# Kernel tuning notes

Hardware: AMD Instinct MI355X
Metric: run time of the kernel (lower is better)

## Reference

```python
import jax, jax.numpy as jnp
import numpy as np

AUG = 8     # augmented_dim
NSUB = 4    # fixed Bosh3 substeps per save interval (replaces adaptive PID controller)


def setup_inputs() -> dict:
    key = jax.random.key(0)
    ks = jax.random.split(key, 8)
    B, T, DATA, WIDTH = 256, 64, 256, 256
    D = DATA + AUG
    ts = jnp.linspace(0.0, 1.0, T, dtype=jnp.float32)
    xs = jax.random.uniform(ks[0], (B, DATA), dtype=jnp.float32)
    a_sample = jax.random.normal(ks[1], (B,), dtype=jnp.float32)

    def lin(k, fan_in, fan_out):
        lim = 1.0 / np.sqrt(fan_in)
        kw, kb = jax.random.split(k)
        W = jax.random.uniform(kw, (fan_out, fan_in), minval=-lim, maxval=lim, dtype=jnp.float32)
        b = jax.random.uniform(kb, (fan_out,), minval=-lim, maxval=lim, dtype=jnp.float32)
        return W, b

    W0, b0 = lin(ks[2], D, WIDTH)
    W1, b1 = lin(ks[3], WIDTH, WIDTH)
    W2, b2 = lin(ks[4], WIDTH, WIDTH)
    W3, b3 = lin(ks[5], WIDTH, D)
    return dict(ts=ts, xs=xs, a_sample=a_sample,
                W0=W0, b0=b0, W1=W1, b1=b1, W2=W2, b2=b2, W3=W3, b3=b3)


def reference(ts, xs, a_sample, W0, b0, W1, b1, W2, b2, W3, b3):
    B = xs.shape[0]

    def f(y):  # autonomous vector field: MLP(y), batched over B
        h = jnp.tanh(y @ W0.T + b0)
        h = jnp.tanh(h @ W1.T + b1)
        h = jnp.tanh(h @ W2.T + b2)
        return h @ W3.T + b3

    # y0 = concat(a * exp(-0.1*t0) * sin(pi*xs), zeros(AUG))
    u0 = jnp.sin(jnp.pi * xs)
    scale = (a_sample * jnp.exp(-0.1 * ts[0]))[:, None]
    y0 = jnp.concatenate([scale * u0, jnp.zeros((B, AUG), xs.dtype)], axis=-1)  # [B, D]

    @jax.checkpoint
    def bosh3_step(y, h):
        k1 = f(y)
        k2 = f(y + 0.5 * h * k1)
        k3 = f(y + 0.75 * h * k2)
        return y + h * ((2.0 / 9.0) * k1 + (1.0 / 3.0) * k2 + (4.0 / 9.0) * k3)

    def interval(y, dt):
        h = dt / NSUB
        y = jax.lax.fori_loop(0, NSUB, lambda i, yy: bosh3_step(yy, h), y)
        return y, y

    dts = ts[1:] - ts[:-1]
    _, ys_tail = jax.lax.scan(interval, y0, dts)             # [T-1, B, D]
    ys = jnp.concatenate([y0[None], ys_tail], axis=0)        # [T, B, D]
    ys = jnp.transpose(ys, (1, 0, 2))[..., :-AUG]            # [B, T, data_size]
    return ys
```

## Files before the change

kernel.cpp:

```cpp
#include <hip/hip_runtime.h>
#include <cmath>

#define NB   256
#define NT   64
#define DATA 256
#define DD   264
#define NSUB 4
#define NTH  1024
#define NW   16
#define PI_F 3.14159265358979323846f

typedef _Float16 h2 __attribute__((ext_vector_type(2)));
typedef __fp16   g2 __attribute__((ext_vector_type(2)));

#define WS_W0  0
#define WS_W1  (WS_W0 + 136 * 256)
#define WS_W2  (WS_W1 + 128 * 256)
#define WS_W3  (WS_W2 + 128 * 256)
#define WS_W3T (WS_W3 + 128 * 256)

#define L_W1   0
#define L_PS   (L_W1 + 128 * 256)
#define L_YP   (L_PS + NW * 272)
#define L_INP  (L_YP + 136)
#define L_HAP  (L_INP + 136)
#define L_HBP  (L_HAP + 128)
#define L_Y    (L_HBP + 128)
#define L_ACC  (L_Y + 272)
#define L_B0   (L_ACC + 272)
#define L_B1   (L_B0 + 256)
#define L_B2   (L_B1 + 256)
#define L_B3   (L_B2 + 256)
#define LDS_WORDS (L_B3 + 272)

__device__ __forceinline__ float dot2(unsigned wu, unsigned hu, float c) {
  h2 a = __builtin_bit_cast(h2, wu);
  h2 b = __builtin_bit_cast(h2, hu);
#if __has_builtin(__builtin_amdgcn_fdot2)
  return __builtin_amdgcn_fdot2(a, b, c, false);
#else
  return c + (float)a[0] * (float)b[0] + (float)a[1] * (float)b[1];
#endif
}

__device__ __forceinline__ unsigned pkh(float a, float b) {
#if __has_builtin(__builtin_amdgcn_cvt_pkrtz)
  g2 v = __builtin_amdgcn_cvt_pkrtz(a, b);
  return __builtin_bit_cast(unsigned, v);
#else
  h2 v; v[0] = (_Float16)a; v[1] = (_Float16)b;
  return __builtin_bit_cast(unsigned, v);
#endif
}

__device__ __forceinline__ unsigned pkh_rne(float a, float b) {
  h2 v; v[0] = (_Float16)a; v[1] = (_Float16)b;
  return __builtin_bit_cast(unsigned, v);
}

#define DOT4(acc, u, hp)                                                      \
  acc.x = dot2(u.x, hp, acc.x);                                               \
  acc.y = dot2(u.y, hp, acc.y);                                               \
  acc.z = dot2(u.z, hp, acc.z);                                               \
  acc.w = dot2(u.w, hp, acc.w);

__global__ void prep(const float* __restrict__ W0, const float* __restrict__ W1,
                     const float* __restrict__ W2, const float* __restrict__ W3,
                     unsigned* __restrict__ wsu) {
  int tid = blockIdx.x * blockDim.x + threadIdx.x;
  int stride = gridDim.x * blockDim.x;
  for (int i = tid; i < 136 * 256; i += stride) {
    int kk = i >> 8, j = i & 255;
    int k0 = 2 * kk, k1 = 2 * kk + 1;
    float lo = (k0 < DD) ? W0[j * DD + k0] : 0.f;
    float hi = (k1 < DD) ? W0[j * DD + k1] : 0.f;
    wsu[WS_W0 + i] = pkh_rne(lo, hi);
  }
  for (int i = tid; i < 128 * 256; i += stride) {
    int kk = i >> 8, j = i & 255;
    wsu[WS_W1 + i] = pkh_rne(W1[j * 256 + 2 * kk], W1[j * 256 + 2 * kk + 1]);
    wsu[WS_W2 + i] = pkh_rne(W2[j * 256 + 2 * kk], W2[j * 256 + 2 * kk + 1]);
    wsu[WS_W3 + i] = pkh_rne(W3[j * 256 + 2 * kk], W3[j * 256 + 2 * kk + 1]);
  }
  for (int i = tid; i < 128 * 16; i += stride) {
    int kk = i >> 4, c = 256 + (i & 15);
    float lo = (c < DD) ? W3[c * 256 + 2 * kk] : 0.f;
    float hi = (c < DD) ? W3[c * 256 + 2 * kk + 1] : 0.f;
    wsu[WS_W3T + i] = pkh_rne(lo, hi);
  }
}

__global__ __launch_bounds__(NTH) void node_integrate(
    const float* __restrict__ ts, const float* __restrict__ xs,
    const float* __restrict__ a_sample,
    const float* __restrict__ b0g, const float* __restrict__ b1g,
    const float* __restrict__ b2g, const float* __restrict__ b3g,
    const unsigned* __restrict__ wsu, float* __restrict__ out) {
  extern __shared__ float sm[];
  unsigned* smu = (unsigned*)sm;
  const int b   = blockIdx.x;
  const int tid = threadIdx.x;
  const int w   = tid >> 6;
  const int l   = tid & 63;

  for (int i = tid; i < 256; i += NTH) {
    sm[L_B0 + i] = b0g[i];
    sm[L_B1 + i] = b1g[i];
    sm[L_B2 + i] = b2g[i];
  }
  for (int i = tid; i < 272; i += NTH) sm[L_B3 + i] = (i < DD) ? b3g[i] : 0.f;
  {
    const uint4* src = (const uint4*)(wsu + WS_W1);
    uint4* dst = (uint4*)(smu + L_W1);
    for (int i = tid; i < 128 * 64; i += NTH) dst[i] = src[i];
  }
  {
    const float sc = a_sample[b] * expf(-0.1f * ts[0]);
    for (int i = tid; i < 272; i += NTH) {
      float v = 0.f;
      if (i < DATA) v = sc * sinf(PI_F * xs[(size_t)b * DATA + i]);
      sm[L_Y + i] = v;
    }
  }
  __syncthreads();
  if (tid < 136) {
    smu[L_YP + tid]  = pkh(sm[L_Y + 2 * tid], sm[L_Y + 2 * tid + 1]);
    smu[L_INP + tid] = 0u;
  }
  __syncthreads();

  if (tid < DATA) out[((size_t)b * NT) * DATA + tid] = sm[L_Y + tid];

  float4* ps4 = (float4*)(sm + L_PS);
  const uint4* w0b4 = (const uint4*)(wsu + WS_W0);
  const uint4* w2b4 = (const uint4*)(wsu + WS_W2);
  const uint4* w3b4 = (const uint4*)(wsu + WS_W3);
  const uint4* w3t4 = (const uint4*)(wsu + WS_W3T);
  const uint4* w1l4 = (const uint4*)(smu + L_W1);

#pragma unroll 1
  for (int t = 0; t < NT - 1; ++t) {
    const float dt = ts[t + 1] - ts[t];
    const float h  = dt * (1.0f / NSUB);
#pragma unroll 1
    for (int sub = 0; sub < NSUB; ++sub) {
#pragma unroll 1
      for (int st = 0; st < 3; ++st) {
        const unsigned* finp = smu + ((st == 0) ? L_YP : L_INP);

        {
          float4 acc; acc.x = acc.y = acc.z = acc.w = 0.f;
#pragma unroll 4
          for (int i = 0; i < 8; ++i) {
            const int kk = w + 16 * i;
            const uint4 u = w0b4[kk * 64 + l];
            const unsigned hp = finp[kk];
            DOT4(acc, u, hp)
          }
          if (w < 8) {
            const int kk = 128 + w;
            const uint4 u = w0b4[kk * 64 + l];
            const unsigned hp = finp[kk];
            DOT4(acc, u, hp)
          }
          ps4[w * 68 + l] = acc;
        }
        __syncthreads();
        if (tid < 256) {
          float sv = sm[L_B0 + tid];
#pragma unroll
          for (int ww = 0; ww < NW; ++ww) sv += sm[L_PS + ww * 272 + tid];
          const float hv = tanhf(sv);
          const float ho = __shfl_xor(hv, 1);
          if (!(tid & 1)) smu[L_HAP + (tid >> 1)] = pkh(hv, ho);
        }
        __syncthreads();

        {
          float4 acc; acc.x = acc.y = acc.z = acc.w = 0.f;
#pragma unroll 4
          for (int i = 0; i < 8; ++i) {
            const int kk = w + 16 * i;
            const uint4 u = w1l4[kk * 64 + l];
            const unsigned hp = smu[L_HAP + kk];
            DOT4(acc, u, hp)
          }
          ps4[w * 68 + l] = acc;
        }
        __syncthreads();
        if (tid < 256) {
          float sv = sm[L_B1 + tid];
#pragma unroll
          for (int ww = 0; ww < NW; ++ww) sv += sm[L_PS + ww * 272 + tid];
          const float hv = tanhf(sv);
          const float ho = __shfl_xor(hv, 1);
          if (!(tid & 1)) smu[L_HBP + (tid >> 1)] = pkh(hv, ho);
        }
        __syncthreads();

        {
          float4 acc; acc.x = acc.y = acc.z = acc.w = 0.f;
#pragma unroll 4
          for (int i = 0; i < 8; ++i) {
            const int kk = w + 16 * i;
            const uint4 u = w2b4[kk * 64 + l];
            const unsigned hp = smu[L_HBP + kk];
            DOT4(acc, u, hp)
          }
          ps4[w * 68 + l] = acc;
        }
        __syncthreads();
        if (tid < 256) {
          float sv = sm[L_B2 + tid];
#pragma unroll
          for (int ww = 0; ww < NW; ++ww) sv += sm[L_PS + ww * 272 + tid];
          const float hv = tanhf(sv);
          const float ho = __shfl_xor(hv, 1);
          if (!(tid & 1)) smu[L_HAP + (tid >> 1)] = pkh(hv, ho);
        }
        __syncthreads();

        {
          float4 acc; acc.x = acc.y = acc.z = acc.w = 0.f;
#pragma unroll 4
          for (int i = 0; i < 8; ++i) {
            const int kk = w + 16 * i;
            const uint4 u = w3b4[kk * 64 + l];
            const unsigned hp = smu[L_HAP + kk];
            DOT4(acc, u, hp)
          }
          ps4[w * 68 + l] = acc;
          if (l < 4) {
            float4 accx; accx.x = accx.y = accx.z = accx.w = 0.f;
#pragma unroll 4
            for (int i = 0; i < 8; ++i) {
              const int kk = w + 16 * i;
              const uint4 u = w3t4[kk * 4 + l];
              const unsigned hp = smu[L_HAP + kk];
              DOT4(accx, u, hp)
            }
            ps4[w * 68 + 64 + l] = accx;
          }
        }
        __syncthreads();
        if (tid < DD) {
          float kv = sm[L_B3 + tid];
#pragma unroll
          for (int ww = 0; ww < NW; ++ww) kv += sm[L_PS + ww * 272 + tid];
          float val;
          if (st == 0) {
            sm[L_ACC + tid] = (2.0f / 9.0f) * kv;
            val = sm[L_Y + tid] + 0.5f * h * kv;
          } else if (st == 1) {
            sm[L_ACC + tid] += (1.0f / 3.0f) * kv;
            val = sm[L_Y + tid] + 0.75f * h * kv;
          } else {
            val = sm[L_Y + tid] + h * (sm[L_ACC + tid] + (4.0f / 9.0f) * kv);
            sm[L_Y + tid] = val;
          }
          const float vo = __shfl_xor(val, 1);
          if (!(tid & 1)) {
            const int dst = (st == 2) ? L_YP : L_INP;
            smu[dst + (tid >> 1)] = pkh(val, vo);
          }
        }
        __syncthreads();
      }
    }
    if (tid < DATA) out[((size_t)b * NT + (t + 1)) * DATA + tid] = sm[L_Y + tid];
  }
}

extern "C" void kernel_launch(void* const* d_in, const int* in_sizes, int n_in,
                              void* d_out, int out_size, void* d_ws, size_t ws_size,
                              hipStream_t stream) {
  const float* ts = (const float*)d_in[0];
  const float* xs = (const float*)d_in[1];
  const float* a  = (const float*)d_in[2];
  const float* W0 = (const float*)d_in[3];
  const float* b0 = (const float*)d_in[4];
  const float* W1 = (const float*)d_in[5];
  const float* b1 = (const float*)d_in[6];
  const float* W2 = (const float*)d_in[7];
  const float* b2 = (const float*)d_in[8];
  const float* W3 = (const float*)d_in[9];
  const float* b3 = (const float*)d_in[10];
  unsigned* ws = (unsigned*)d_ws;
  float* out = (float*)d_out;

  const size_t lds_bytes = LDS_WORDS * sizeof(float);
  (void)hipFuncSetAttribute(reinterpret_cast<const void*>(node_integrate),
                            hipFuncAttributeMaxDynamicSharedMemorySize,
                            (int)lds_bytes);

  hipLaunchKernelGGL(prep, dim3(256), dim3(256), 0, stream, W0, W1, W2, W3, ws);
  hipLaunchKernelGGL(node_integrate, dim3(NB), dim3(NTH), lds_bytes, stream,
                     ts, xs, a, b0, b1, b2, b3, ws, out);
}
```

Baseline: 4.697 ms.

## Keep ODE state in registers and align each wave's K-slice to its own outputs

Each wave now reduces the outputs it will consume as the K-slice of the next layer, so the tanh-and-pack step no longer needs a block-wide barrier. This roughly halves __syncthreads per MLP evaluation. Partial sums are double-buffered between two LDS regions. The RK state (y, acc) and biases move into registers, and the augmented tail is handled by a small separate path. To make room in LDS, the last rows of W1 are now read from global memory. That adds some global traffic and branching in the W1 loop.

```diff
diff --git a/kernel.cpp b/kernel.cpp
--- a/kernel.cpp
+++ b/kernel.cpp
@@ -7,7 +7,6 @@
 #define DD   264
 #define NSUB 4
 #define NTH  1024
-#define NW   16
 #define PI_F 3.14159265358979323846f
 
 typedef _Float16 h2 __attribute__((ext_vector_type(2)));
@@ -19,19 +18,13 @@
 #define WS_W3  (WS_W2 + 128 * 256)
 #define WS_W3T (WS_W3 + 128 * 256)
 
+#define NW1LDS 124
 #define L_W1   0
-#define L_PS   (L_W1 + 128 * 256)
-#define L_YP   (L_PS + NW * 272)
-#define L_INP  (L_YP + 136)
-#define L_HAP  (L_INP + 136)
-#define L_HBP  (L_HAP + 128)
-#define L_Y    (L_HBP + 128)
-#define L_ACC  (L_Y + 272)
-#define L_B0   (L_ACC + 272)
-#define L_B1   (L_B0 + 256)
-#define L_B2   (L_B1 + 256)
-#define L_B3   (L_B2 + 256)
-#define LDS_WORDS (L_B3 + 272)
+#define L_PSA  (L_W1 + NW1LDS * 256)
+#define L_PSB  (L_PSA + 16 * 256)
+#define L_PT   (L_PSB + 16 * 256)
+#define L_FPH  (L_PT + 16 * 8)
+#define LDS_WORDS (L_FPH + 16 * 9)
 
 __device__ __forceinline__ float dot2(unsigned wu, unsigned hu, float c) {
   h2 a = __builtin_bit_cast(h2, wu);
@@ -42,7 +35,6 @@
   return c + (float)a[0] * (float)b[0] + (float)a[1] * (float)b[1];
 #endif
 }
-
 __device__ __forceinline__ unsigned pkh(float a, float b) {
 #if __has_builtin(__builtin_amdgcn_cvt_pkrtz)
   g2 v = __builtin_amdgcn_cvt_pkrtz(a, b);
@@ -52,7 +44,6 @@
   return __builtin_bit_cast(unsigned, v);
 #endif
 }
-
 __device__ __forceinline__ unsigned pkh_rne(float a, float b) {
   h2 v; v[0] = (_Float16)a; v[1] = (_Float16)b;
   return __builtin_bit_cast(unsigned, v);
@@ -82,11 +73,9 @@
     wsu[WS_W2 + i] = pkh_rne(W2[j * 256 + 2 * kk], W2[j * 256 + 2 * kk + 1]);
     wsu[WS_W3 + i] = pkh_rne(W3[j * 256 + 2 * kk], W3[j * 256 + 2 * kk + 1]);
   }
-  for (int i = tid; i < 128 * 16; i += stride) {
-    int kk = i >> 4, c = 256 + (i & 15);
-    float lo = (c < DD) ? W3[c * 256 + 2 * kk] : 0.f;
-    float hi = (c < DD) ? W3[c * 256 + 2 * kk + 1] : 0.f;
-    wsu[WS_W3T + i] = pkh_rne(lo, hi);
+  for (int i = tid; i < 128 * 8; i += stride) {
+    int kk = i >> 3, c = 256 + (i & 7);
+    wsu[WS_W3T + i] = pkh_rne(W3[c * 256 + 2 * kk], W3[c * 256 + 2 * kk + 1]);
   }
 }
 
@@ -96,178 +85,185 @@
     const float* __restrict__ b0g, const float* __restrict__ b1g,
     const float* __restrict__ b2g, const float* __restrict__ b3g,
     const unsigned* __restrict__ wsu, float* __restrict__ out) {
-  extern __shared__ float sm[];
-  unsigned* smu = (unsigned*)sm;
-  const int b   = blockIdx.x;
+  HIP_DYNAMIC_SHARED(unsigned, sm);
+  float* smf = (float*)sm;
+  const int b = blockIdx.x;
   const int tid = threadIdx.x;
-  const int w   = tid >> 6;
-  const int l   = tid & 63;
-
-  for (int i = tid; i < 256; i += NTH) {
-    sm[L_B0 + i] = b0g[i];
-    sm[L_B1 + i] = b1g[i];
-    sm[L_B2 + i] = b2g[i];
-  }
-  for (int i = tid; i < 272; i += NTH) sm[L_B3 + i] = (i < DD) ? b3g[i] : 0.f;
+  const int w = tid >> 6, l = tid & 63;
+  const int g = l >> 2, s = l & 3;
+  const int jg = 16 * w + g;
+
   {
     const uint4* src = (const uint4*)(wsu + WS_W1);
-    uint4* dst = (uint4*)(smu + L_W1);
-    for (int i = tid; i < 128 * 64; i += NTH) dst[i] = src[i];
-  }
+    uint4* dst = (uint4*)(sm + L_W1);
+    for (int i = tid; i < NW1LDS * 64; i += NTH) dst[i] = src[i];
+  }
+  const float rb0 = b0g[jg], rb1 = b1g[jg], rb2 = b2g[jg], rb3 = b3g[jg];
+  const int jt = 256 + 2 * w + (l >> 2);
+  const float rb3t = (w < 4 && l < 8) ? b3g[jt] : 0.f;
+
+  const float sc = a_sample[b] * expf(-0.1f * ts[0]);
+  float y_g = sc * sinf(PI_F * xs[(size_t)b * DATA + jg]);
+  float acc_g = 0.f, fv = y_g;
+  float y_t = 0.f, acc_t = 0.f, fvt = 0.f;
+
   {
-    const float sc = a_sample[b] * expf(-0.1f * ts[0]);
-    for (int i = tid; i < 272; i += NTH) {
-      float v = 0.f;
-      if (i < DATA) v = sc * sinf(PI_F * xs[(size_t)b * DATA + i]);
-      sm[L_Y + i] = v;
-    }
+    const float fo = __shfl_xor(fv, 4);
+    if ((l & 7) == 0) sm[L_FPH + w * 9 + (l >> 3)] = pkh(fv, fo);
+    if (l == 0) sm[L_FPH + w * 9 + 8] = 0u;
   }
   __syncthreads();
-  if (tid < 136) {
-    smu[L_YP + tid]  = pkh(sm[L_Y + 2 * tid], sm[L_Y + 2 * tid + 1]);
-    smu[L_INP + tid] = 0u;
-  }
-  __syncthreads();
-
-  if (tid < DATA) out[((size_t)b * NT) * DATA + tid] = sm[L_Y + tid];
-
-  float4* ps4 = (float4*)(sm + L_PS);
+  if (s == 0) out[((size_t)b * NT) * DATA + jg] = y_g;
+
   const uint4* w0b4 = (const uint4*)(wsu + WS_W0);
+  const uint4* w1g4 = (const uint4*)(wsu + WS_W1);
   const uint4* w2b4 = (const uint4*)(wsu + WS_W2);
   const uint4* w3b4 = (const uint4*)(wsu + WS_W3);
   const uint4* w3t4 = (const uint4*)(wsu + WS_W3T);
-  const uint4* w1l4 = (const uint4*)(smu + L_W1);
+  const uint4* w1l4 = (const uint4*)(sm + L_W1);
 
 #pragma unroll 1
   for (int t = 0; t < NT - 1; ++t) {
     const float dt = ts[t + 1] - ts[t];
-    const float h  = dt * (1.0f / NSUB);
+    const float h = dt * (1.0f / NSUB);
 #pragma unroll 1
     for (int sub = 0; sub < NSUB; ++sub) {
 #pragma unroll 1
       for (int st = 0; st < 3; ++st) {
-        const unsigned* finp = smu + ((st == 0) ? L_YP : L_INP);
-
-        {
-          float4 acc; acc.x = acc.y = acc.z = acc.w = 0.f;
-#pragma unroll 4
-          for (int i = 0; i < 8; ++i) {
-            const int kk = w + 16 * i;
+        {
+          float4 acc; acc.x = acc.y = acc.z = acc.w = 0.f;
+#pragma unroll 4
+          for (int i = 0; i < 8; ++i) {
+            const int kk = 8 * w + i;
             const uint4 u = w0b4[kk * 64 + l];
-            const unsigned hp = finp[kk];
-            DOT4(acc, u, hp)
-          }
-          if (w < 8) {
+            const unsigned hp = sm[L_FPH + w * 9 + i];
+            DOT4(acc, u, hp)
+          }
+          if (w < 4) {
             const int kk = 128 + w;
             const uint4 u = w0b4[kk * 64 + l];
-            const unsigned hp = finp[kk];
-            DOT4(acc, u, hp)
-          }
-          ps4[w * 68 + l] = acc;
-        }
-        __syncthreads();
-        if (tid < 256) {
-          float sv = sm[L_B0 + tid];
-#pragma unroll
-          for (int ww = 0; ww < NW; ++ww) sv += sm[L_PS + ww * 272 + tid];
-          const float hv = tanhf(sv);
-          const float ho = __shfl_xor(hv, 1);
-          if (!(tid & 1)) smu[L_HAP + (tid >> 1)] = pkh(hv, ho);
-        }
-        __syncthreads();
-
-        {
-          float4 acc; acc.x = acc.y = acc.z = acc.w = 0.f;
-#pragma unroll 4
-          for (int i = 0; i < 8; ++i) {
-            const int kk = w + 16 * i;
-            const uint4 u = w1l4[kk * 64 + l];
-            const unsigned hp = smu[L_HAP + kk];
-            DOT4(acc, u, hp)
-          }
-          ps4[w * 68 + l] = acc;
-        }
-        __syncthreads();
-        if (tid < 256) {
-          float sv = sm[L_B1 + tid];
-#pragma unroll
-          for (int ww = 0; ww < NW; ++ww) sv += sm[L_PS + ww * 272 + tid];
-          const float hv = tanhf(sv);
-          const float ho = __shfl_xor(hv, 1);
-          if (!(tid & 1)) smu[L_HBP + (tid >> 1)] = pkh(hv, ho);
-        }
-        __syncthreads();
-
-        {
-          float4 acc; acc.x = acc.y = acc.z = acc.w = 0.f;
-#pragma unroll 4
-          for (int i = 0; i < 8; ++i) {
-            const int kk = w + 16 * i;
+            const unsigned hp = sm[L_FPH + w * 9 + 8];
+            DOT4(acc, u, hp)
+          }
+          ((float4*)(smf + L_PSA + w * 256))[l] = acc;
+        }
+        __syncthreads();
+        {
+          float sv = 0.f;
+#pragma unroll
+          for (int p = s; p < 16; p += 4) sv += smf[L_PSA + p * 256 + jg];
+          sv += __shfl_xor(sv, 1); sv += __shfl_xor(sv, 2);
+          const float hv = tanhf(sv + rb0);
+          const float ho = __shfl_xor(hv, 4);
+          if ((l & 7) == 0) sm[L_FPH + w * 9 + (l >> 3)] = pkh(hv, ho);
+        }
+        {
+          float4 acc; acc.x = acc.y = acc.z = acc.w = 0.f;
+#pragma unroll 4
+          for (int i = 0; i < 8; ++i) {
+            const int kk = 8 * w + i;
+            uint4 u;
+            if (kk < NW1LDS) u = w1l4[kk * 64 + l];
+            else             u = w1g4[kk * 64 + l];
+            const unsigned hp = sm[L_FPH + w * 9 + i];
+            DOT4(acc, u, hp)
+          }
+          ((float4*)(smf + L_PSB + w * 256))[l] = acc;
+        }
+        __syncthreads();
+        {
+          float sv = 0.f;
+#pragma unroll
+          for (int p = s; p < 16; p += 4) sv += smf[L_PSB + p * 256 + jg];
+          sv += __shfl_xor(sv, 1); sv += __shfl_xor(sv, 2);
+          const float hv = tanhf(sv + rb1);
+          const float ho = __shfl_xor(hv, 4);
+          if ((l & 7) == 0) sm[L_FPH + w * 9 + (l >> 3)] = pkh(hv, ho);
+        }
+        {
+          float4 acc; acc.x = acc.y = acc.z = acc.w = 0.f;
+#pragma unroll 4
+          for (int i = 0; i < 8; ++i) {
+            const int kk = 8 * w + i;
             const uint4 u = w2b4[kk * 64 + l];
-            const unsigned hp = smu[L_HBP + kk];
-            DOT4(acc, u, hp)
-          }
-          ps4[w * 68 + l] = acc;
-        }
-        __syncthreads();
-        if (tid < 256) {
-          float sv = sm[L_B2 + tid];
-#pragma unroll
-          for (int ww = 0; ww < NW; ++ww) sv += sm[L_PS + ww * 272 + tid];
-          const float hv = tanhf(sv);
-          const float ho = __shfl_xor(hv, 1);
-          if (!(tid & 1)) smu[L_HAP + (tid >> 1)] = pkh(hv, ho);
-        }
-        __syncthreads();
-
-        {
-          float4 acc; acc.x = acc.y = acc.z = acc.w = 0.f;
-#pragma unroll 4
-          for (int i = 0; i < 8; ++i) {
-            const int kk = w + 16 * i;
+            const unsigned hp = sm[L_FPH + w * 9 + i];
+            DOT4(acc, u, hp)
+          }
+          ((float4*)(smf + L_PSA + w * 256))[l] = acc;
+        }
+        __syncthreads();
+        {
+          float sv = 0.f;
+#pragma unroll
+          for (int p = s; p < 16; p += 4) sv += smf[L_PSA + p * 256 + jg];
+          sv += __shfl_xor(sv, 1); sv += __shfl_xor(sv, 2);
+          const float hv = tanhf(sv + rb2);
+          const float ho = __shfl_xor(hv, 4);
+          if ((l & 7) == 0) sm[L_FPH + w * 9 + (l >> 3)] = pkh(hv, ho);
+        }
+        {
+          float4 acc; acc.x = acc.y = acc.z = acc.w = 0.f;
+#pragma unroll 4
+          for (int i = 0; i < 8; ++i) {
+            const int kk = 8 * w + i;
             const uint4 u = w3b4[kk * 64 + l];
-            const unsigned hp = smu[L_HAP + kk];
-            DOT4(acc, u, hp)
-          }
-          ps4[w * 68 + l] = acc;
-          if (l < 4) {
+            const unsigned hp = sm[L_FPH + w * 9 + i];
+            DOT4(acc, u, hp)
+          }
+          ((float4*)(smf + L_PSB + w * 256))[l] = acc;
+          if (l < 2) {
             float4 accx; accx.x = accx.y = accx.z = accx.w = 0.f;
 #pragma unroll 4
             for (int i = 0; i < 8; ++i) {
-              const int kk = w + 16 * i;
-              const uint4 u = w3t4[kk * 4 + l];
-              const unsigned hp = smu[L_HAP + kk];
+              const int kk = 8 * w + i;
+              const uint4 u = w3t4[kk * 2 + l];
+              const unsigned hp = sm[L_FPH + w * 9 + i];
               DOT4(accx, u, hp)
             }
-            ps4[w * 68 + 64 + l] = accx;
-          }
-        }
-        __syncthreads();
-        if (tid < DD) {
-          float kv = sm[L_B3 + tid];
-#pragma unroll
-          for (int ww = 0; ww < NW; ++ww) kv += sm[L_PS + ww * 272 + tid];
-          float val;
+            ((float4*)(smf + L_PT + w * 8))[l] = accx;
+          }
+        }
+        __syncthreads();
+        {
+          float sv = 0.f;
+#pragma unroll
+          for (int p = s; p < 16; p += 4) sv += smf[L_PSB + p * 256 + jg];
+          sv += __shfl_xor(sv, 1); sv += __shfl_xor(sv, 2);
+          const float kv = sv + rb3;
+          float svt = 0.f;
+          if (w < 4 && l < 8) {
+#pragma unroll
+            for (int tt = 0; tt < 4; ++tt) {
+              const int p = (l & 3) + 4 * tt;
+              svt += smf[L_PT + p * 8 + 2 * w + (l >> 2)];
+            }
+          }
+          svt += __shfl_xor(svt, 1); svt += __shfl_xor(svt, 2);
+          const float kvt = svt + rb3t;
           if (st == 0) {
-            sm[L_ACC + tid] = (2.0f / 9.0f) * kv;
-            val = sm[L_Y + tid] + 0.5f * h * kv;
+            acc_g = (2.0f / 9.0f) * kv;
+            fv = y_g + 0.5f * h * kv;
+            acc_t = (2.0f / 9.0f) * kvt;
+            fvt = y_t + 0.5f * h * kvt;
           } else if (st == 1) {
-            sm[L_ACC + tid] += (1.0f / 3.0f) * kv;
-            val = sm[L_Y + tid] + 0.75f * h * kv;
+            acc_g += (1.0f / 3.0f) * kv;
+            fv = y_g + 0.75f * h * kv;
+            acc_t += (1.0f / 3.0f) * kvt;
+            fvt = y_t + 0.75f * h * kvt;
           } else {
-            val = sm[L_Y + tid] + h * (sm[L_ACC + tid] + (4.0f / 9.0f) * kv);
-            sm[L_Y + tid] = val;
-          }
-          const float vo = __shfl_xor(val, 1);
-          if (!(tid & 1)) {
-            const int dst = (st == 2) ? L_YP : L_INP;
-            smu[dst + (tid >> 1)] = pkh(val, vo);
-          }
-        }
-        __syncthreads();
+            y_g += h * (acc_g + (4.0f / 9.0f) * kv);
+            fv = y_g;
+            y_t += h * (acc_t + (4.0f / 9.0f) * kvt);
+            fvt = y_t;
+          }
+          const float fo = __shfl_xor(fv, 4);
+          if ((l & 7) == 0) sm[L_FPH + w * 9 + (l >> 3)] = pkh(fv, fo);
+          const float fot = __shfl_xor(fvt, 4);
+          if (l == 0) sm[L_FPH + w * 9 + 8] = (w < 4) ? pkh(fvt, fot) : 0u;
+        }
       }
     }
-    if (tid < DATA) out[((size_t)b * NT + (t + 1)) * DATA + tid] = sm[L_Y + tid];
+    if (s == 0) out[((size_t)b * NT + (t + 1)) * DATA + jg] = y_g;
   }
 }
 
@@ -288,7 +284,7 @@
   unsigned* ws = (unsigned*)d_ws;
   float* out = (float*)d_out;
 
-  const size_t lds_bytes = LDS_WORDS * sizeof(float);
+  const size_t lds_bytes = LDS_WORDS * sizeof(unsigned);
   (void)hipFuncSetAttribute(reinterpret_cast<const void*>(node_integrate),
                             hipFuncAttributeMaxDynamicSharedMemorySize,
                             (int)lds_bytes);
```

Result: slower. 5.207 ms (+10.9%).
